# Kernel optimization log

Hardware: AMD Instinct MI355X
Metric: run time of the kernel (lower is better)

Reference implementation:

```python
import jax, jax.numpy as jnp
import numpy as np

B, S, N, H, NH = 2, 2048, 1024, 1024, 16
D = H // NH  # head dim = 64


def setup_inputs() -> dict:
    key = jax.random.key(0)
    ks = jax.random.split(key, 7)
    scale = 1.0 / np.sqrt(H)
    return {
        "token_q": jax.random.normal(ks[0], (B, S, H), dtype=jnp.float32),
        "block_kv": jax.random.normal(ks[1], (B, N, H), dtype=jnp.float32),
        "block_ends": jnp.sort(jax.random.randint(ks[2], (N,), 0, S, dtype=jnp.int32)),
        "Wq": jax.random.normal(ks[3], (H, H), dtype=jnp.float32) * scale,
        "Wk": jax.random.normal(ks[4], (H, H), dtype=jnp.float32) * scale,
        "Wv": jax.random.normal(ks[5], (H, H), dtype=jnp.float32) * scale,
        "Wo": jax.random.normal(ks[6], (H, H), dtype=jnp.float32) * scale,
    }


def reference(token_q, block_kv, block_ends, Wq, Wk, Wv, Wo):
    # nn.Linear: y = x @ W.T (no bias)
    q = (token_q @ Wq.T).reshape(B, S, NH, D).transpose(0, 2, 1, 3)   # [B,h,S,d]
    k = (block_kv @ Wk.T).reshape(B, N, NH, D).transpose(0, 2, 1, 3)  # [B,h,N,d]
    v = (block_kv @ Wv.T).reshape(B, N, NH, D).transpose(0, 2, 1, 3)  # [B,h,N,d]

    attn = jnp.einsum("bhsd,bhnd->bhsn", q, k) / jnp.sqrt(jnp.float32(D))

    # strict_causal mask: block is visible iff its end position <= query index t
    t_idx = jnp.arange(S, dtype=block_ends.dtype)[:, None]           # [S,1]
    mask = block_ends[None, :] <= t_idx                               # [S,N]
    neg = jnp.finfo(attn.dtype).min
    attn = jnp.where(mask[None, None, :, :], attn, neg)

    attn = jax.nn.softmax(attn, axis=-1)
    out = jnp.einsum("bhsn,bhnd->bhsd", attn, v)                      # [B,h,S,d]
    out = out.transpose(0, 2, 1, 3).reshape(B, S, H)
    return out @ Wo.T
```

## Files before the change

kernel.cpp:

```cpp
#include <hip/hip_runtime.h>
#include <float.h>
#include <stdint.h>

#define B_  2
#define S_  2048
#define N_  1024
#define H_  1024
#define NH_ 16
#define K_  1024

typedef __attribute__((ext_vector_type(8))) short bf16x8;
typedef __attribute__((ext_vector_type(4))) float f32x4;

typedef __attribute__((address_space(3))) uint32_t lds_u32;
typedef __attribute__((address_space(1))) uint32_t glb_u32;

__device__ __forceinline__ void gload16(void* l, const void* g) {
    __builtin_amdgcn_global_load_lds((const glb_u32*)g, (lds_u32*)l, 16, 0, 0);
}

__device__ __forceinline__ ushort f2bf(float f) {
    uint32_t u = __float_as_uint(f);
    u = (u + 0x7fffu + ((u >> 16) & 1u)) >> 16;
    return (ushort)u;
}

#if __has_builtin(__builtin_amdgcn_cvt_pk_bf16_f32)
typedef __attribute__((ext_vector_type(2))) __bf16 bfp2;
__device__ __forceinline__ uint pk2(float a, float b) {
    bfp2 v = __builtin_amdgcn_cvt_pk_bf16_f32(a, b);
    return __builtin_bit_cast(uint, v);
}
#else
__device__ __forceinline__ uint pk2(float a, float b) {
    return (uint)f2bf(a) | ((uint)f2bf(b) << 16);
}
#endif

__device__ __forceinline__ float fexp2(float x) {
#if __has_builtin(__builtin_amdgcn_exp2f)
    return __builtin_amdgcn_exp2f(x);
#else
    return exp2f(x);
#endif
}

#define SC2 0.180336880f

__global__ __launch_bounds__(256) void prep_kernel(const float* __restrict__ tq,
        const float* __restrict__ kv, const float* __restrict__ wq,
        const float* __restrict__ wk, const float* __restrict__ wv,
        const float* __restrict__ wo, ushort* __restrict__ dst)
{
    int blk = blockIdx.x;
    const float* src; size_t base;
    if (blk < 2048)      { src = tq; base = 0;       }
    else if (blk < 3072) { src = kv; base = 4194304; blk -= 2048; }
    else if (blk < 3584) { src = wq; base = 6291456; blk -= 3072; }
    else if (blk < 4096) { src = wk; base = 7340032; blk -= 3584; }
    else if (blk < 4608) { src = wv; base = 8388608; blk -= 4096; }
    else                 { src = wo; base = 9437184; blk -= 4608; }
    size_t i = (size_t)blk * 2048 + threadIdx.x * 8;
    float4 a = *(const float4*)(src + i);
    float4 b = *(const float4*)(src + i + 4);
    uint4 o;
    o.x = pk2(a.x, a.y); o.y = pk2(a.z, a.w);
    o.z = pk2(b.x, b.y); o.w = pk2(b.z, b.w);
    *(uint4*)(dst + base + i) = o;
}

__global__ __launch_bounds__(512) void gemm_qkv(
        const ushort* __restrict__ qx, const ushort* __restrict__ kvx,
        const ushort* __restrict__ wq, const ushort* __restrict__ wk,
        const ushort* __restrict__ wv,
        ushort* __restrict__ Qp, ushort* __restrict__ Kp,
        ushort* __restrict__ VtG, float* __restrict__ VmP)
{
    __shared__ __align__(16) ushort smem[17408];
    ushort* Xs = smem;
    ushort* Ws = smem + 8192;

    const ushort* X; const ushort* W; void* Yp; int kind; float scale = 1.f;
    int bm, bn;
    {
        int idx = blockIdx.x;
        if (idx < 256)      { X = qx;  W = wq; Yp = Qp;  kind = 0; scale = SC2;
                              bm = (idx >> 3) * 128; bn = (idx & 7) * 128; }
        else if (idx < 384) { int j = idx - 256; X = kvx; W = wk; Yp = Kp; kind = 0;
                              bm = (j >> 3) * 128; bn = (j & 7) * 128; }
        else                { int j = idx - 384; X = kvx; W = wv; Yp = VtG; kind = 2;
                              bm = (j >> 3) * 128; bn = (j & 7) * 128; }
    }

    const int tid = threadIdx.x;
    const int lane = tid & 63, w = tid >> 6;
    const int wy = w >> 1, wx = w & 1;
    const int c = lane & 15, g = lane >> 4;

    f32x4 acc[2][4] = {};

    for (int kt = 0; kt < 16; ++kt) {
        const int k0 = kt * 64;
#pragma unroll
        for (int j = 0; j < 2; ++j) {
            int u = w * 128 + j * 64 + lane;
            int row = u >> 3, gs = (u & 7) ^ (row & 7);
            gload16(Xs + (w * 128 + j * 64) * 8, X + (size_t)(bm + row) * K_ + k0 + gs * 8);
            gload16(Ws + (w * 128 + j * 64) * 8, W + (size_t)(bn + row) * K_ + k0 + gs * 8);
        }
        __syncthreads();
#pragma unroll
        for (int ks = 0; ks < 2; ++ks) {
            bf16x8 af[2], bfr[4];
#pragma unroll
            for (int mi = 0; mi < 2; ++mi) {
                int row = wy * 32 + mi * 16 + c;
                int s = ks * 4 + g;
                af[mi] = *(const bf16x8*)(Xs + (row * 8 + (s ^ (row & 7))) * 8);
            }
#pragma unroll
            for (int ni = 0; ni < 4; ++ni) {
                int row = wx * 64 + ni * 16 + c;
                int s = ks * 4 + g;
                bfr[ni] = *(const bf16x8*)(Ws + (row * 8 + (s ^ (row & 7))) * 8);
            }
#pragma unroll
            for (int mi = 0; mi < 2; ++mi)
#pragma unroll
                for (int ni = 0; ni < 4; ++ni)
                    acc[mi][ni] = __builtin_amdgcn_mfma_f32_16x16x32_bf16(af[mi], bfr[ni], acc[mi][ni], 0, 0, 0);
        }
        __syncthreads();
    }

    if (kind == 0) {
        ushort* Y = (ushort*)Yp;
#pragma unroll
        for (int mi = 0; mi < 2; ++mi)
#pragma unroll
            for (int ni = 0; ni < 4; ++ni)
#pragma unroll
                for (int r = 0; r < 4; ++r) {
                    int row = bm + wy * 32 + mi * 16 + g * 4 + r;
                    int col = bn + wx * 64 + ni * 16 + c;
                    Y[(size_t)row * 1024 + col] = f2bf(acc[mi][ni][r] * scale);
                }
    } else {
        ushort* T = smem;
#pragma unroll
        for (int mi = 0; mi < 2; ++mi)
#pragma unroll
            for (int ni = 0; ni < 4; ++ni) {
                ushort4 v4;
                v4.x = f2bf(acc[mi][ni][0]); v4.y = f2bf(acc[mi][ni][1]);
                v4.z = f2bf(acc[mi][ni][2]); v4.w = f2bf(acc[mi][ni][3]);
                *(ushort4*)&T[(wx * 64 + ni * 16 + c) * 136 + wy * 32 + mi * 16 + g * 4] = v4;
            }
        __syncthreads();
        ushort* Vt = (ushort*)Yp;
        int b = bm >> 10;
        int rid = tid >> 2, quad = tid & 3;
        int n_c = bn + rid;
        int h = n_c >> 6, d = n_c & 63;
        int m0 = quad * 32;
        ushort* dst = Vt + (size_t)((b * NH_ + h) * 64 + d) * N_ + (bm & (N_ - 1)) + m0;
        float vsum = 0.f;
#pragma unroll
        for (int jj = 0; jj < 4; ++jj) {
            uint4 tt = *(const uint4*)&T[rid * 136 + m0 + jj * 8];
            *(uint4*)(dst + jj * 8) = tt;
            uint uu[4] = {tt.x, tt.y, tt.z, tt.w};
#pragma unroll
            for (int q2 = 0; q2 < 4; ++q2) {
                vsum += __uint_as_float(uu[q2] << 16);
                vsum += __uint_as_float(uu[q2] & 0xffff0000u);
            }
        }
        vsum += __shfl_xor(vsum, 1);
        vsum += __shfl_xor(vsum, 2);
        if (quad == 0) VmP[(bm >> 7) * 1024 + n_c] = vsum;
    }
}

__global__ __launch_bounds__(256) void attn_mfma(const ushort* __restrict__ Qp,
                                                 const ushort* __restrict__ Kp,
                                                 const ushort* __restrict__ VtG,
                                                 const int* __restrict__ ends,
                                                 const float* __restrict__ VmP,
                                                 ushort* __restrict__ AO)
{
    __shared__ __align__(16) ushort Qs[128 * 64];
    __shared__ __align__(16) ushort Ks[64 * 64];
    __shared__ __align__(16) ushort Vs[64 * 64];
    __shared__ __align__(16) ushort Ps[128][72];
    __shared__ int cntS[128];

    const int id = blockIdx.x;
    const int b = id & 1, h = (id >> 1) & 15;
    const int tb = id >> 5;
    const int t0 = (tb < 8 ? tb : 23 - tb) << 7;
    const int tid = threadIdx.x, lane = tid & 63, w = tid >> 6;
    const int c = lane & 15, g = lane >> 4;

#pragma unroll
    for (int jj = 0; jj < 4; ++jj) {
        int u = w * 256 + jj * 64 + lane;
        int row = u >> 3, gs = (u & 7) ^ (row & 7);
        gload16(Qs + (w * 256 + jj * 64) * 8,
                Qp + (size_t)(b * S_ + t0 + row) * H_ + h * 64 + gs * 8);
    }
    if (tid < 128) {
        int t = t0 + tid;
        int lo = 0, hi = N_;
        while (lo < hi) { int mid = (lo + hi) >> 1; if (ends[mid] <= t) lo = mid + 1; else hi = mid; }
        cntS[tid] = lo;
    }

    const int u0 = (w * 2) * 64 + lane, row0 = u0 >> 3, gs0 = (u0 & 7) ^ (row0 & 7);
    const int u1 = (w * 2 + 1) * 64 + lane, row1 = u1 >> 3, gs1 = (u1 & 7) ^ (row1 & 7);
    const ushort* kp0 = Kp + (size_t)(b * N_ + row0) * H_ + h * 64 + gs0 * 8;
    const ushort* kp1 = Kp + (size_t)(b * N_ + row1) * H_ + h * 64 + gs1 * 8;
    const ushort* vp0 = VtG + (size_t)((b * NH_ + h) * 64 + row0) * N_ + gs0 * 8;
    const ushort* vp1 = VtG + (size_t)((b * NH_ + h) * 64 + row1) * N_ + gs1 * 8;

    float l0 = 0.f, l1 = 0.f;
    f32x4 o0[4] = {}, o1[4] = {};

    __syncthreads();
    const int cntv0 = cntS[w * 32 + c];
    const int cntv1 = cntS[w * 32 + 16 + c];
    const int cnt_min = cntS[0];
    const int ntmax = (cntS[127] + 63) >> 6;

    bf16x8 bq0[2], bq1[2];
#pragma unroll
    for (int ks = 0; ks < 2; ++ks) {
        int s = ks * 4 + g;
        int ra = w * 32 + c;
        bq0[ks] = *(const bf16x8*)(Qs + (ra * 8 + (s ^ (ra & 7))) * 8);
        int rb = w * 32 + 16 + c;
        bq1[ks] = *(const bf16x8*)(Qs + (rb * 8 + (s ^ (rb & 7))) * 8);
    }

    for (int nt = 0; nt < ntmax; ++nt) {
        gload16(Ks + (w * 2) * 512, kp0 + (size_t)nt * 64 * H_);
        gload16(Ks + (w * 2 + 1) * 512, kp1 + (size_t)nt * 64 * H_);
        gload16(Vs + (w * 2) * 512, vp0 + nt * 64);
        gload16(Vs + (w * 2 + 1) * 512, vp1 + nt * 64);
        __syncthreads();

        f32x4 st0[4] = {}, st1[4] = {};
#pragma unroll
        for (int ntile = 0; ntile < 4; ++ntile)
#pragma unroll
            for (int ks = 0; ks < 2; ++ks) {
                int row = ntile * 16 + c;
                int s = ks * 4 + g;
                bf16x8 ak = *(const bf16x8*)(Ks + (row * 8 + (s ^ (row & 7))) * 8);
                st0[ntile] = __builtin_amdgcn_mfma_f32_16x16x32_bf16(ak, bq0[ks], st0[ntile], 0, 0, 0);
                st1[ntile] = __builtin_amdgcn_mfma_f32_16x16x32_bf16(ak, bq1[ks], st1[ntile], 0, 0, 0);
            }

        const bool full = ((nt + 1) << 6) <= cnt_min;
        float lsum0 = 0.f, lsum1 = 0.f;
        if (full) {
#pragma unroll
            for (int ntile = 0; ntile < 4; ++ntile) {
                float a0 = fexp2(st0[ntile][0]), a1 = fexp2(st0[ntile][1]);
                float a2 = fexp2(st0[ntile][2]), a3 = fexp2(st0[ntile][3]);
                lsum0 += (a0 + a1) + (a2 + a3);
                uint2 pw; pw.x = pk2(a0, a1); pw.y = pk2(a2, a3);
                *(uint2*)&Ps[w * 32 + c][ntile * 16 + g * 4] = pw;
                float b0 = fexp2(st1[ntile][0]), b1 = fexp2(st1[ntile][1]);
                float b2 = fexp2(st1[ntile][2]), b3 = fexp2(st1[ntile][3]);
                lsum1 += (b0 + b1) + (b2 + b3);
                uint2 qw; qw.x = pk2(b0, b1); qw.y = pk2(b2, b3);
                *(uint2*)&Ps[w * 32 + 16 + c][ntile * 16 + g * 4] = qw;
            }
        } else {
            const int base0 = (nt << 6) + g * 4 - cntv0;
            const int base1 = (nt << 6) + g * 4 - cntv1;
#pragma unroll
            for (int ntile = 0; ntile < 4; ++ntile) {
                float a0 = (base0 + ntile * 16 + 0 >= 0) ? 0.f : fexp2(st0[ntile][0]);
                float a1 = (base0 + ntile * 16 + 1 >= 0) ? 0.f : fexp2(st0[ntile][1]);
                float a2 = (base0 + ntile * 16 + 2 >= 0) ? 0.f : fexp2(st0[ntile][2]);
                float a3 = (base0 + ntile * 16 + 3 >= 0) ? 0.f : fexp2(st0[ntile][3]);
                lsum0 += (a0 + a1) + (a2 + a3);
                uint2 pw; pw.x = pk2(a0, a1); pw.y = pk2(a2, a3);
                *(uint2*)&Ps[w * 32 + c][ntile * 16 + g * 4] = pw;
                float b0 = (base1 + ntile * 16 + 0 >= 0) ? 0.f : fexp2(st1[ntile][0]);
                float b1 = (base1 + ntile * 16 + 1 >= 0) ? 0.f : fexp2(st1[ntile][1]);
                float b2 = (base1 + ntile * 16 + 2 >= 0) ? 0.f : fexp2(st1[ntile][2]);
                float b3 = (base1 + ntile * 16 + 3 >= 0) ? 0.f : fexp2(st1[ntile][3]);
                lsum1 += (b0 + b1) + (b2 + b3);
                uint2 qw; qw.x = pk2(b0, b1); qw.y = pk2(b2, b3);
                *(uint2*)&Ps[w * 32 + 16 + c][ntile * 16 + g * 4] = qw;
            }
        }
        lsum0 += __shfl_xor(lsum0, 16); lsum0 += __shfl_xor(lsum0, 32);
        lsum1 += __shfl_xor(lsum1, 16); lsum1 += __shfl_xor(lsum1, 32);
        l0 += lsum0; l1 += lsum1;

        bf16x8 ap0[2], ap1[2];
#pragma unroll
        for (int ks = 0; ks < 2; ++ks) {
            ap0[ks] = *(const bf16x8*)&Ps[w * 32 + c][ks * 32 + g * 8];
            ap1[ks] = *(const bf16x8*)&Ps[w * 32 + 16 + c][ks * 32 + g * 8];
        }
#pragma unroll
        for (int dt = 0; dt < 4; ++dt)
#pragma unroll
            for (int ks = 0; ks < 2; ++ks) {
                int row = dt * 16 + c;
                int s = ks * 4 + g;
                bf16x8 bv = *(const bf16x8*)(Vs + (row * 8 + (s ^ (row & 7))) * 8);
                o0[dt] = __builtin_amdgcn_mfma_f32_16x16x32_bf16(ap0[ks], bv, o0[dt], 0, 0, 0);
                o1[dt] = __builtin_amdgcn_mfma_f32_16x16x32_bf16(ap1[ks], bv, o1[dt], 0, 0, 0);
            }
        __syncthreads();
    }

#pragma unroll
    for (int qt = 0; qt < 2; ++qt) {
        float invl = 1.f / (qt == 0 ? l0 : l1);
        f32x4* o = (qt == 0 ? o0 : o1);
        float lr[4]; int cq[4];
#pragma unroll
        for (int r = 0; r < 4; ++r) {
            lr[r] = __shfl(invl, g * 4 + r);
            cq[r] = cntS[w * 32 + qt * 16 + g * 4 + r];
        }
#pragma unroll
        for (int dt = 0; dt < 4; ++dt)
#pragma unroll
            for (int r = 0; r < 4; ++r) {
                int q = t0 + w * 32 + qt * 16 + g * 4 + r;
                float val = o[dt][r] * lr[r];
                if (cq[r] == 0) {
                    float sm = 0.f;
#pragma unroll
                    for (int j = 0; j < 8; ++j)
                        sm += VmP[(b * 8 + j) * 1024 + h * 64 + dt * 16 + c];
                    val = sm * (1.f / 1024.f);
                }
                AO[(size_t)(b * S_ + q) * H_ + h * 64 + dt * 16 + c] = f2bf(val);
            }
    }
}

__global__ __launch_bounds__(512) void gemm_out(const ushort* __restrict__ AO,
                                                const ushort* __restrict__ wo,
                                                float* __restrict__ out)
{
    __shared__ __align__(16) ushort Xs[64 * 64];
    __shared__ __align__(16) ushort Ws[128 * 64];

    const int bm = (blockIdx.x >> 3) * 64;
    const int bn = (blockIdx.x & 7) * 128;
    const int tid = threadIdx.x, lane = tid & 63, w = tid >> 6;
    const int wy = w >> 2, wx = w & 3;
    const int c = lane & 15, g = lane >> 4;

    const int rx = tid >> 3,          sx = (tid & 7) ^ (rx & 7);
    const int rw0 = tid >> 3,         sw0 = (tid & 7) ^ (rw0 & 7);
    const int uw1 = tid + 512;
    const int rw1 = uw1 >> 3,         sw1 = (uw1 & 7) ^ (rw1 & 7);

    const ushort* xp  = AO + (size_t)(bm + rx) * K_ + sx * 8;
    const ushort* wp0 = wo + (size_t)(bn + rw0) * K_ + sw0 * 8;
    const ushort* wp1 = wo + (size_t)(bn + rw1) * K_ + sw1 * 8;

    f32x4 acc[2][2] = {};

    for (int kt = 0; kt < 16; ++kt) {
        const int k0 = kt * 64;
        gload16(Xs + (w * 64) * 8, xp + k0);
        gload16(Ws + (w * 64) * 8, wp0 + k0);
        gload16(Ws + (512 + w * 64) * 8, wp1 + k0);
        __syncthreads();
#pragma unroll
        for (int ks = 0; ks < 2; ++ks) {
            bf16x8 af[2], bfr[2];
            int s = ks * 4 + g;
#pragma unroll
            for (int mi = 0; mi < 2; ++mi) {
                int row = wy * 32 + mi * 16 + c;
                af[mi] = *(const bf16x8*)(Xs + (row * 8 + (s ^ (row & 7))) * 8);
            }
#pragma unroll
            for (int ni = 0; ni < 2; ++ni) {
                int row = wx * 32 + ni * 16 + c;
                bfr[ni] = *(const bf16x8*)(Ws + (row * 8 + (s ^ (row & 7))) * 8);
            }
#pragma unroll
            for (int mi = 0; mi < 2; ++mi)
#pragma unroll
                for (int ni = 0; ni < 2; ++ni)
                    acc[mi][ni] = __builtin_amdgcn_mfma_f32_16x16x32_bf16(af[mi], bfr[ni], acc[mi][ni], 0, 0, 0);
        }
        __syncthreads();
    }

#pragma unroll
    for (int mi = 0; mi < 2; ++mi)
#pragma unroll
        for (int ni = 0; ni < 2; ++ni)
#pragma unroll
            for (int r = 0; r < 4; ++r) {
                int row = bm + wy * 32 + mi * 16 + g * 4 + r;
                int col = bn + wx * 32 + ni * 16 + c;
                out[(size_t)row * 1024 + col] = acc[mi][ni][r];
            }
}

extern "C" void kernel_launch(void* const* d_in, const int* in_sizes, int n_in,
                              void* d_out, int out_size, void* d_ws, size_t ws_size,
                              hipStream_t stream) {
    const float* token_q    = (const float*)d_in[0];
    const float* block_kv   = (const float*)d_in[1];
    const int*   block_ends = (const int*)d_in[2];
    const float* Wq = (const float*)d_in[3];
    const float* Wk = (const float*)d_in[4];
    const float* Wv = (const float*)d_in[5];
    const float* Wo = (const float*)d_in[6];
    float* out = (float*)d_out;

    ushort* ws  = (ushort*)d_ws;
    ushort* qx  = ws;
    ushort* kvx = ws + (size_t)4 * 1024 * 1024;
    ushort* wqb = ws + (size_t)6 * 1024 * 1024;
    ushort* wkb = ws + (size_t)7 * 1024 * 1024;
    ushort* wvb = ws + (size_t)8 * 1024 * 1024;
    ushort* wob = ws + (size_t)9 * 1024 * 1024;
    ushort* Qp  = ws + (size_t)10 * 1024 * 1024;
    ushort* Kp  = ws + (size_t)14 * 1024 * 1024;
    ushort* VtG = ws + (size_t)16 * 1024 * 1024;
    float*  VmP = (float*)(ws + (size_t)18 * 1024 * 1024);

    prep_kernel<<<5120, 256, 0, stream>>>(token_q, block_kv, Wq, Wk, Wv, Wo, ws);
    gemm_qkv<<<512, 512, 0, stream>>>(qx, kvx, wqb, wkb, wvb, Qp, Kp, VtG, VmP);
    attn_mfma<<<512, 256, 0, stream>>>(Qp, Kp, VtG, block_ends, VmP, Qp);
    gemm_out<<<512, 512, 0, stream>>>(Qp, wob, out);
}
```

Before: 159.1 us.

## Fuse all four stages into one cooperative persistent kernel with grid syncs

Replaces the four separate launches (convert, QKV GEMM, attention, output GEMM) with a single cooperative kernel of 256 blocks of 512 threads that loops over the work tiles and uses grid.sync between stages. The goal is to remove kernel launch gaps and tail effects between stages. Each block now handles two tiles per stage, with fewer waves in flight and grid-wide barriers. The attention stage pairs tiles j and 15-j to balance causal work. The old multi-kernel path is kept as a fallback if the cooperative launch fails.

New measurement: 459.5 us. +188.8%, slower.

```diff
diff --git a/kernel.cpp b/kernel.cpp
--- a/kernel.cpp
+++ b/kernel.cpp
@@ -1,6 +1,9 @@
 #include <hip/hip_runtime.h>
+#include <hip/hip_cooperative_groups.h>
 #include <float.h>
 #include <stdint.h>
+
+namespace cg = cooperative_groups;
 
 #define B_  2
 #define S_  2048
@@ -46,6 +49,351 @@
 }
 
 #define SC2 0.180336880f
+
+__global__ __launch_bounds__(512, 2) void mega(
+        const float* __restrict__ tqF, const float* __restrict__ kvF,
+        const float* __restrict__ wqF, const float* __restrict__ wkF,
+        const float* __restrict__ wvF, const float* __restrict__ woF,
+        const int* __restrict__ ends, ushort* __restrict__ ws,
+        float* __restrict__ out)
+{
+    __shared__ __align__(16) ushort smem[25856];
+    cg::grid_group grid = cg::this_grid();
+
+    ushort* qx  = ws;
+    ushort* kvx = ws + 4194304;
+    ushort* wq  = ws + 6291456;
+    ushort* wk  = ws + 7340032;
+    ushort* wv  = ws + 8388608;
+    ushort* wo  = ws + 9437184;
+    ushort* Qp  = ws + 10485760;
+    ushort* Kp  = ws + 14680064;
+    ushort* VtG = ws + 16777216;
+    float*  VmP = (float*)(ws + 18874368);
+    ushort* AO  = ws + 20971520;
+
+    const int tid = threadIdx.x;
+    const int bid = blockIdx.x;
+    const int lane = tid & 63, w = tid >> 6;
+    const int c = lane & 15, g = lane >> 4;
+
+#pragma unroll
+    for (int i = 0; i < 10; ++i) {
+        size_t off = (size_t)(i * 256 + bid) * 4096 + tid * 8;
+        const float* src; size_t base;
+        if (off < 4194304)      { src = tqF; base = 0; }
+        else if (off < 6291456) { src = kvF; base = 4194304; }
+        else if (off < 7340032) { src = wqF; base = 6291456; }
+        else if (off < 8388608) { src = wkF; base = 7340032; }
+        else if (off < 9437184) { src = wvF; base = 8388608; }
+        else                    { src = woF; base = 9437184; }
+        const float* s = src + (off - base);
+        float4 a = *(const float4*)s;
+        float4 b = *(const float4*)(s + 4);
+        uint4 o;
+        o.x = pk2(a.x, a.y); o.y = pk2(a.z, a.w);
+        o.z = pk2(b.x, b.y); o.w = pk2(b.z, b.w);
+        *(uint4*)(ws + off) = o;
+    }
+    __threadfence();
+    grid.sync();
+
+    for (int uu = 0; uu < 2; ++uu) {
+        __syncthreads();
+        ushort* Xs = smem;
+        ushort* WsL = smem + 8192;
+
+        int idx = bid + uu * 256;
+        const ushort* X; const ushort* W; ushort* Yp; int kind; float scale = 1.f;
+        int bm, bn;
+        if (idx < 256)      { X = qx;  W = wq; Yp = Qp;  kind = 0; scale = SC2;
+                              bm = (idx >> 3) * 128; bn = (idx & 7) * 128; }
+        else if (idx < 384) { int j = idx - 256; X = kvx; W = wk; Yp = Kp; kind = 0;
+                              bm = (j >> 3) * 128; bn = (j & 7) * 128; }
+        else                { int j = idx - 384; X = kvx; W = wv; Yp = VtG; kind = 2;
+                              bm = (j >> 3) * 128; bn = (j & 7) * 128; }
+
+        const int wy = w >> 1, wx = w & 1;
+        f32x4 acc[2][4] = {};
+
+        for (int kt = 0; kt < 16; ++kt) {
+            const int k0 = kt * 64;
+#pragma unroll
+            for (int j = 0; j < 2; ++j) {
+                int u = w * 128 + j * 64 + lane;
+                int row = u >> 3, gs = (u & 7) ^ (row & 7);
+                gload16(Xs + (w * 128 + j * 64) * 8, X + (size_t)(bm + row) * K_ + k0 + gs * 8);
+                gload16(WsL + (w * 128 + j * 64) * 8, W + (size_t)(bn + row) * K_ + k0 + gs * 8);
+            }
+            __syncthreads();
+#pragma unroll
+            for (int ks = 0; ks < 2; ++ks) {
+                bf16x8 af[2], bfr[4];
+#pragma unroll
+                for (int mi = 0; mi < 2; ++mi) {
+                    int row = wy * 32 + mi * 16 + c;
+                    int s = ks * 4 + g;
+                    af[mi] = *(const bf16x8*)(Xs + (row * 8 + (s ^ (row & 7))) * 8);
+                }
+#pragma unroll
+                for (int ni = 0; ni < 4; ++ni) {
+                    int row = wx * 64 + ni * 16 + c;
+                    int s = ks * 4 + g;
+                    bfr[ni] = *(const bf16x8*)(WsL + (row * 8 + (s ^ (row & 7))) * 8);
+                }
+#pragma unroll
+                for (int mi = 0; mi < 2; ++mi)
+#pragma unroll
+                    for (int ni = 0; ni < 4; ++ni)
+                        acc[mi][ni] = __builtin_amdgcn_mfma_f32_16x16x32_bf16(af[mi], bfr[ni], acc[mi][ni], 0, 0, 0);
+            }
+            __syncthreads();
+        }
+
+        if (kind == 0) {
+#pragma unroll
+            for (int mi = 0; mi < 2; ++mi)
+#pragma unroll
+                for (int ni = 0; ni < 4; ++ni)
+#pragma unroll
+                    for (int r = 0; r < 4; ++r) {
+                        int row = bm + wy * 32 + mi * 16 + g * 4 + r;
+                        int col = bn + wx * 64 + ni * 16 + c;
+                        Yp[(size_t)row * 1024 + col] = f2bf(acc[mi][ni][r] * scale);
+                    }
+        } else {
+            ushort* T = smem;
+#pragma unroll
+            for (int mi = 0; mi < 2; ++mi)
+#pragma unroll
+                for (int ni = 0; ni < 4; ++ni) {
+                    ushort4 v4;
+                    v4.x = f2bf(acc[mi][ni][0]); v4.y = f2bf(acc[mi][ni][1]);
+                    v4.z = f2bf(acc[mi][ni][2]); v4.w = f2bf(acc[mi][ni][3]);
+                    *(ushort4*)&T[(wx * 64 + ni * 16 + c) * 136 + wy * 32 + mi * 16 + g * 4] = v4;
+                }
+            __syncthreads();
+            int b = bm >> 10;
+            int rid = tid >> 2, quad = tid & 3;
+            int n_c = bn + rid;
+            int h = n_c >> 6, d = n_c & 63;
+            int m0 = quad * 32;
+            ushort* dst = Yp + (size_t)((b * NH_ + h) * 64 + d) * N_ + (bm & (N_ - 1)) + m0;
+            float vsum = 0.f;
+#pragma unroll
+            for (int jj = 0; jj < 4; ++jj) {
+                uint4 tt = *(const uint4*)&T[rid * 136 + m0 + jj * 8];
+                *(uint4*)(dst + jj * 8) = tt;
+                uint uw[4] = {tt.x, tt.y, tt.z, tt.w};
+#pragma unroll
+                for (int q2 = 0; q2 < 4; ++q2) {
+                    vsum += __uint_as_float(uw[q2] << 16);
+                    vsum += __uint_as_float(uw[q2] & 0xffff0000u);
+                }
+            }
+            vsum += __shfl_xor(vsum, 1);
+            vsum += __shfl_xor(vsum, 2);
+            if (quad == 0) VmP[(bm >> 7) * 1024 + n_c] = vsum;
+        }
+    }
+    __threadfence();
+    grid.sync();
+
+    for (int uu = 0; uu < 2; ++uu) {
+        __syncthreads();
+        ushort* Qs = smem;
+        ushort* Ks = smem + 8192;
+        ushort* Vs = smem + 12288;
+        ushort* Ps = smem + 16384;
+        int* cntS  = (int*)(smem + 25600);
+
+        const int m = bid >> 5, k2 = bid & 31;
+        const int j = (uu == 0) ? m : 15 - m;
+        const int b = k2 & 1, h = k2 >> 1;
+        const int t0 = j << 7;
+
+#pragma unroll
+        for (int jj = 0; jj < 2; ++jj) {
+            int u = w * 128 + jj * 64 + lane;
+            int row = u >> 3, gs = (u & 7) ^ (row & 7);
+            gload16(Qs + (w * 128 + jj * 64) * 8,
+                    Qp + (size_t)(b * S_ + t0 + row) * H_ + h * 64 + gs * 8);
+        }
+        if (tid < 128) {
+            int t = t0 + tid;
+            int lo = 0, hi = N_;
+            while (lo < hi) { int mid = (lo + hi) >> 1; if (ends[mid] <= t) lo = mid + 1; else hi = mid; }
+            cntS[tid] = lo;
+        }
+
+        const int u0 = w * 64 + lane, row0 = u0 >> 3, gs0 = (u0 & 7) ^ (row0 & 7);
+        const ushort* kp0 = Kp + (size_t)(b * N_ + row0) * H_ + h * 64 + gs0 * 8;
+        const ushort* vp0 = VtG + (size_t)((b * NH_ + h) * 64 + row0) * N_ + gs0 * 8;
+
+        float l0 = 0.f;
+        f32x4 o0[4] = {};
+
+        __syncthreads();
+        const int cntv = cntS[w * 16 + c];
+        const int cnt_min = cntS[0];
+        const int ntmax = (cntS[127] + 63) >> 6;
+
+        bf16x8 bq[2];
+#pragma unroll
+        for (int ks = 0; ks < 2; ++ks) {
+            int ra = w * 16 + c;
+            int s = ks * 4 + g;
+            bq[ks] = *(const bf16x8*)(Qs + (ra * 8 + (s ^ (ra & 7))) * 8);
+        }
+
+        for (int nt = 0; nt < ntmax; ++nt) {
+            gload16(Ks + w * 512, kp0 + (size_t)nt * 64 * H_);
+            gload16(Vs + w * 512, vp0 + nt * 64);
+            __syncthreads();
+
+            f32x4 st[4] = {};
+#pragma unroll
+            for (int ntile = 0; ntile < 4; ++ntile)
+#pragma unroll
+                for (int ks = 0; ks < 2; ++ks) {
+                    int row = ntile * 16 + c;
+                    int s = ks * 4 + g;
+                    bf16x8 ak = *(const bf16x8*)(Ks + (row * 8 + (s ^ (row & 7))) * 8);
+                    st[ntile] = __builtin_amdgcn_mfma_f32_16x16x32_bf16(ak, bq[ks], st[ntile], 0, 0, 0);
+                }
+
+            const bool full = ((nt + 1) << 6) <= cnt_min;
+            float lsum = 0.f;
+            ushort* prow = Ps + (size_t)(w * 16 + c) * 72;
+            if (full) {
+#pragma unroll
+                for (int ntile = 0; ntile < 4; ++ntile) {
+                    float a0 = fexp2(st[ntile][0]), a1 = fexp2(st[ntile][1]);
+                    float a2 = fexp2(st[ntile][2]), a3 = fexp2(st[ntile][3]);
+                    lsum += (a0 + a1) + (a2 + a3);
+                    uint2 pw; pw.x = pk2(a0, a1); pw.y = pk2(a2, a3);
+                    *(uint2*)(prow + ntile * 16 + g * 4) = pw;
+                }
+            } else {
+                const int base = (nt << 6) + g * 4 - cntv;
+#pragma unroll
+                for (int ntile = 0; ntile < 4; ++ntile) {
+                    float a0 = (base + ntile * 16 + 0 >= 0) ? 0.f : fexp2(st[ntile][0]);
+                    float a1 = (base + ntile * 16 + 1 >= 0) ? 0.f : fexp2(st[ntile][1]);
+                    float a2 = (base + ntile * 16 + 2 >= 0) ? 0.f : fexp2(st[ntile][2]);
+                    float a3 = (base + ntile * 16 + 3 >= 0) ? 0.f : fexp2(st[ntile][3]);
+                    lsum += (a0 + a1) + (a2 + a3);
+                    uint2 pw; pw.x = pk2(a0, a1); pw.y = pk2(a2, a3);
+                    *(uint2*)(prow + ntile * 16 + g * 4) = pw;
+                }
+            }
+            lsum += __shfl_xor(lsum, 16);
+            lsum += __shfl_xor(lsum, 32);
+            l0 += lsum;
+
+            bf16x8 ap[2];
+#pragma unroll
+            for (int ks = 0; ks < 2; ++ks)
+                ap[ks] = *(const bf16x8*)(prow + ks * 32 + g * 8);
+#pragma unroll
+            for (int dt = 0; dt < 4; ++dt)
+#pragma unroll
+                for (int ks = 0; ks < 2; ++ks) {
+                    int row = dt * 16 + c;
+                    int s = ks * 4 + g;
+                    bf16x8 bv = *(const bf16x8*)(Vs + (row * 8 + (s ^ (row & 7))) * 8);
+                    o0[dt] = __builtin_amdgcn_mfma_f32_16x16x32_bf16(ap[ks], bv, o0[dt], 0, 0, 0);
+                }
+            __syncthreads();
+        }
+
+        float invl = 1.f / l0;
+        float lr[4]; int cq[4];
+#pragma unroll
+        for (int r = 0; r < 4; ++r) {
+            lr[r] = __shfl(invl, g * 4 + r);
+            cq[r] = cntS[w * 16 + g * 4 + r];
+        }
+#pragma unroll
+        for (int dt = 0; dt < 4; ++dt)
+#pragma unroll
+            for (int r = 0; r < 4; ++r) {
+                int q = t0 + w * 16 + g * 4 + r;
+                float val = o0[dt][r] * lr[r];
+                if (cq[r] == 0) {
+                    float sm = 0.f;
+#pragma unroll
+                    for (int jj = 0; jj < 8; ++jj)
+                        sm += VmP[(b * 8 + jj) * 1024 + h * 64 + dt * 16 + c];
+                    val = sm * (1.f / 1024.f);
+                }
+                AO[(size_t)(b * S_ + q) * H_ + h * 64 + dt * 16 + c] = f2bf(val);
+            }
+    }
+    __threadfence();
+    grid.sync();
+
+    for (int uu = 0; uu < 2; ++uu) {
+        __syncthreads();
+        ushort* Xs = smem;
+        ushort* WsL = smem + 4096;
+
+        int idx = bid + uu * 256;
+        const int bm = (idx >> 3) * 64;
+        const int bn = (idx & 7) * 128;
+        const int wy = w >> 2, wx = w & 3;
+
+        const int rx = tid >> 3,  sx = (tid & 7) ^ (rx & 7);
+        const int uw1 = tid + 512;
+        const int rw1 = uw1 >> 3, sw1 = (uw1 & 7) ^ (rw1 & 7);
+
+        const ushort* xp  = AO + (size_t)(bm + rx) * K_ + sx * 8;
+        const ushort* wp0 = wo + (size_t)(bn + rx) * K_ + sx * 8;
+        const ushort* wp1 = wo + (size_t)(bn + rw1) * K_ + sw1 * 8;
+
+        f32x4 acc[2][2] = {};
+
+        for (int kt = 0; kt < 16; ++kt) {
+            const int k0 = kt * 64;
+            gload16(Xs + (w * 64) * 8, xp + k0);
+            gload16(WsL + (w * 64) * 8, wp0 + k0);
+            gload16(WsL + (512 + w * 64) * 8, wp1 + k0);
+            __syncthreads();
+#pragma unroll
+            for (int ks = 0; ks < 2; ++ks) {
+                bf16x8 af[2], bfr[2];
+                int s = ks * 4 + g;
+#pragma unroll
+                for (int mi = 0; mi < 2; ++mi) {
+                    int row = wy * 32 + mi * 16 + c;
+                    af[mi] = *(const bf16x8*)(Xs + (row * 8 + (s ^ (row & 7))) * 8);
+                }
+#pragma unroll
+                for (int ni = 0; ni < 2; ++ni) {
+                    int row = wx * 32 + ni * 16 + c;
+                    bfr[ni] = *(const bf16x8*)(WsL + (row * 8 + (s ^ (row & 7))) * 8);
+                }
+#pragma unroll
+                for (int mi = 0; mi < 2; ++mi)
+#pragma unroll
+                    for (int ni = 0; ni < 2; ++ni)
+                        acc[mi][ni] = __builtin_amdgcn_mfma_f32_16x16x32_bf16(af[mi], bfr[ni], acc[mi][ni], 0, 0, 0);
+            }
+            __syncthreads();
+        }
+
+#pragma unroll
+        for (int mi = 0; mi < 2; ++mi)
+#pragma unroll
+            for (int ni = 0; ni < 2; ++ni)
+#pragma unroll
+                for (int r = 0; r < 4; ++r) {
+                    int row = bm + wy * 32 + mi * 16 + g * 4 + r;
+                    int col = bn + wx * 32 + ni * 16 + c;
+                    out[(size_t)row * 1024 + col] = acc[mi][ni][r];
+                }
+    }
+}
 
 __global__ __launch_bounds__(256) void prep_kernel(const float* __restrict__ tq,
         const float* __restrict__ kv, const float* __restrict__ wq,
@@ -169,11 +517,11 @@
         for (int jj = 0; jj < 4; ++jj) {
             uint4 tt = *(const uint4*)&T[rid * 136 + m0 + jj * 8];
             *(uint4*)(dst + jj * 8) = tt;
-            uint uu[4] = {tt.x, tt.y, tt.z, tt.w};
+            uint uw[4] = {tt.x, tt.y, tt.z, tt.w};
 #pragma unroll
             for (int q2 = 0; q2 < 4; ++q2) {
-                vsum += __uint_as_float(uu[q2] << 16);
-                vsum += __uint_as_float(uu[q2] & 0xffff0000u);
+                vsum += __uint_as_float(uw[q2] << 16);
+                vsum += __uint_as_float(uw[q2] & 0xffff0000u);
             }
         }
         vsum += __shfl_xor(vsum, 1);
@@ -362,13 +710,12 @@
     const int wy = w >> 2, wx = w & 3;
     const int c = lane & 15, g = lane >> 4;
 
-    const int rx = tid >> 3,          sx = (tid & 7) ^ (rx & 7);
-    const int rw0 = tid >> 3,         sw0 = (tid & 7) ^ (rw0 & 7);
+    const int rx = tid >> 3,  sx = (tid & 7) ^ (rx & 7);
     const int uw1 = tid + 512;
-    const int rw1 = uw1 >> 3,         sw1 = (uw1 & 7) ^ (rw1 & 7);
+    const int rw1 = uw1 >> 3, sw1 = (uw1 & 7) ^ (rw1 & 7);
 
     const ushort* xp  = AO + (size_t)(bm + rx) * K_ + sx * 8;
-    const ushort* wp0 = wo + (size_t)(bn + rw0) * K_ + sw0 * 8;
+    const ushort* wp0 = wo + (size_t)(bn + rx) * K_ + sx * 8;
     const ushort* wp1 = wo + (size_t)(bn + rw1) * K_ + sw1 * 8;
 
     f32x4 acc[2][2] = {};
@@ -425,21 +772,30 @@
     const float* Wv = (const float*)d_in[5];
     const float* Wo = (const float*)d_in[6];
     float* out = (float*)d_out;
-
-    ushort* ws  = (ushort*)d_ws;
-    ushort* qx  = ws;
-    ushort* kvx = ws + (size_t)4 * 1024 * 1024;
-    ushort* wqb = ws + (size_t)6 * 1024 * 1024;
-    ushort* wkb = ws + (size_t)7 * 1024 * 1024;
-    ushort* wvb = ws + (size_t)8 * 1024 * 1024;
-    ushort* wob = ws + (size_t)9 * 1024 * 1024;
-    ushort* Qp  = ws + (size_t)10 * 1024 * 1024;
-    ushort* Kp  = ws + (size_t)14 * 1024 * 1024;
-    ushort* VtG = ws + (size_t)16 * 1024 * 1024;
-    float*  VmP = (float*)(ws + (size_t)18 * 1024 * 1024);
-
-    prep_kernel<<<5120, 256, 0, stream>>>(token_q, block_kv, Wq, Wk, Wv, Wo, ws);
-    gemm_qkv<<<512, 512, 0, stream>>>(qx, kvx, wqb, wkb, wvb, Qp, Kp, VtG, VmP);
-    attn_mfma<<<512, 256, 0, stream>>>(Qp, Kp, VtG, block_ends, VmP, Qp);
-    gemm_out<<<512, 512, 0, stream>>>(Qp, wob, out);
-}
+    ushort* ws = (ushort*)d_ws;
+
+    void* args[] = {
+        (void*)&token_q, (void*)&block_kv,
+        (void*)&Wq, (void*)&Wk, (void*)&Wv, (void*)&Wo,
+        (void*)&block_ends, (void*)&ws, (void*)&out
+    };
+    hipError_t err = hipLaunchCooperativeKernel((const void*)mega, dim3(256),
+                                                dim3(512), args, 0, stream);
+    if (err != hipSuccess) {
+        ushort* qx  = ws;
+        ushort* kvx = ws + (size_t)4 * 1024 * 1024;
+        ushort* wqb = ws + (size_t)6 * 1024 * 1024;
+        ushort* wkb = ws + (size_t)7 * 1024 * 1024;
+        ushort* wvb = ws + (size_t)8 * 1024 * 1024;
+        ushort* wob = ws + (size_t)9 * 1024 * 1024;
+        ushort* Qp  = ws + (size_t)10 * 1024 * 1024;
+        ushort* Kp  = ws + (size_t)14 * 1024 * 1024;
+        ushort* VtG = ws + (size_t)16 * 1024 * 1024;
+        float*  VmP = (float*)(ws + (size_t)18 * 1024 * 1024);
+
+        prep_kernel<<<5120, 256, 0, stream>>>(token_q, block_kv, Wq, Wk, Wv, Wo, ws);
+        gemm_qkv<<<512, 512, 0, stream>>>(qx, kvx, wqb, wkb, wvb, Qp, Kp, VtG, VmP);
+        attn_mfma<<<512, 256, 0, stream>>>(Qp, Kp, VtG, block_ends, VmP, Qp);
+        gemm_out<<<512, 512, 0, stream>>>(Qp, wob, out);
+    }
+}
```
